# Optimization experiments

Hardware: AMD Instinct MI355X
Metric: run time of the kernel (lower is better)

## Reference

```python
import jax, jax.numpy as jnp
import numpy as np

B, C, L, E = 2048, 128, 16, 10      # atoms, channels, num_ell=(lmax+1)^2, elements
P3, P2, P1 = 23, 4, 1               # num CG paths per correlation order
U_DENSITY = 0.15                    # CG-like U tensors are highly sparse


def _sparse_u(key, shape):
    k1, k2 = jax.random.split(key)
    vals = jax.random.normal(k1, shape, dtype=jnp.float32)
    mask = jax.random.uniform(k2, shape) < U_DENSITY
    return jnp.where(mask, vals, 0.0)


def setup_inputs() -> dict:
    key = jax.random.key(0)
    ks = jax.random.split(key, 8)
    x = jax.random.normal(ks[0], (B, C, L), dtype=jnp.float32)
    y = jax.random.uniform(ks[1], (B, E), dtype=jnp.float32)  # element attrs
    U3 = _sparse_u(ks[2], (L, L, L, P3))
    U2 = _sparse_u(ks[3], (L, L, P2))
    U1 = _sparse_u(ks[4], (L, P1))
    W3 = jax.random.normal(ks[5], (E, P3, C), dtype=jnp.float32) / P3
    W2 = jax.random.normal(ks[6], (E, P2, C), dtype=jnp.float32) / P2
    W1 = jax.random.normal(ks[7], (E, P1, C), dtype=jnp.float32) / P1
    return {"x": x, "y": y, "U3": U3, "U2": U2, "U1": U1,
            "W3": W3, "W2": W2, "W1": W1}


def reference(x, y, U3, U2, U1, W3, W2, W1):
    # nu=3 main contraction: 'wxik,ekc,bci,be->bcwx'
    out = jnp.einsum('wxik,ekc,bci,be->bcwx', U3, W3, x, y, optimize='optimal')  # [B,C,L,L]
    # nu=2: weighting then feature contraction
    c2 = jnp.einsum('wxk,ekc,be->bcwx', U2, W2, y, optimize='optimal') + out
    out = jnp.einsum('bcwi,bci->bcw', c2, x)                                     # [B,C,L]
    # nu=1
    c1 = jnp.einsum('wk,ekc,be->bcw', U1, W1, y, optimize='optimal') + out
    out = jnp.einsum('bci,bci->bc', c1, x)                                       # [B,C]
    return out.reshape(out.shape[0], -1)
```

## Files before the change

kernel.cpp:

```cpp
#include <hip/hip_runtime.h>
#include <hip/hip_bf16.h>

typedef __attribute__((ext_vector_type(8))) short short8;
typedef __attribute__((ext_vector_type(4))) float f32x4;

#define LL 16
#define NP3 23
#define NE 10
#define NC 128
#define KI 24
#define KTOT 384
#define NSTEPS 12
#define MT 64
#define THREADS 512
#define WAVES 8
#define ZPAD 392

__global__ void build_B(const float* __restrict__ U3, const float* __restrict__ U2,
                        __hip_bfloat16* __restrict__ Bf) {
    int s    = blockIdx.x >> 4;
    int n16  = blockIdx.x & 15;
    int lane = threadIdx.x;
    int ar   = lane & 15, kg = lane >> 4;
    int n    = n16 * 16 + ar;
    __hip_bfloat16 vals[8];
#pragma unroll
    for (int j = 0; j < 8; ++j) {
        int kk = s * 32 + kg * 8 + j;
        int i  = kk / KI, k = kk - i * KI;
        float v;
        if (k < NP3)      v = U3[((size_t)n * LL + i) * NP3 + k];
        else if (i < 4)   v = U2[n * 4 + i];
        else              v = 0.f;
        vals[j] = __float2bfloat16(v);
    }
    *reinterpret_cast<short8*>(Bf + ((size_t)blockIdx.x * 64 + lane) * 8) =
        *reinterpret_cast<short8*>(vals);
}

__global__ __launch_bounds__(THREADS, 4)
void contract_k(const float* __restrict__ x, const float* __restrict__ y,
                const float* __restrict__ W3, const float* __restrict__ W2,
                const float* __restrict__ W1, const float* __restrict__ U1,
                const __hip_bfloat16* __restrict__ Bf, float* __restrict__ out) {
    __shared__ __align__(16) __hip_bfloat16 Zt[MT][ZPAD];
    __shared__ float xs[MT][17];
    __shared__ float wys[MT][28];
    __shared__ float part[MT][WAVES];

    const int tid = threadIdx.x;
    const int m0  = blockIdx.x * MT;

    for (int idx = tid; idx < MT * LL; idx += THREADS) {
        xs[idx >> 4][idx & 15] = x[(size_t)m0 * LL + idx];
    }

    {
        int r = tid >> 3, p = tid & 7;
        int m = m0 + r;
        int c = m & (NC - 1);
        const float* yr = y + (size_t)(m >> 7) * NE;
        float yv[NE];
#pragma unroll
        for (int e = 0; e < NE; ++e) yv[e] = yr[e];
#pragma unroll
        for (int j = 0; j < 4; ++j) {
            int idx = p * 4 + j;
            if (idx < 28) {
                float s = 0.f;
                if (idx < NP3) {
#pragma unroll
                    for (int e = 0; e < NE; ++e) s += yv[e] * W3[(e * NP3 + idx) * NC + c];
                } else if (idx < 27) {
                    int k2 = idx - NP3;
#pragma unroll
                    for (int e = 0; e < NE; ++e) s += yv[e] * W2[(e * 4 + k2) * NC + c];
                } else {
#pragma unroll
                    for (int e = 0; e < NE; ++e) s += yv[e] * W1[e * NC + c];
                }
                wys[r][idx] = s;
            }
        }
    }
    __syncthreads();

    {
        int r = tid >> 3, p = tid & 7;
        float wv[NP3];
#pragma unroll
        for (int k = 0; k < NP3; ++k) wv[k] = wys[r][k];
#pragma unroll
        for (int ii = 0; ii < 2; ++ii) {
            int i = p * 2 + ii;
            float xi   = xs[r][i];
            float slot = (i < 4) ? wys[r][NP3 + i] : 0.f;
            __hip_bfloat162* dst = reinterpret_cast<__hip_bfloat162*>(&Zt[r][i * KI]);
#pragma unroll
            for (int kp = 0; kp < 12; ++kp) {
                float a = xi * wv[2 * kp];
                float b = (kp < 11) ? xi * wv[2 * kp + 1] : slot;
                __hip_bfloat162 pk;
                pk.x = __float2bfloat16(a);
                pk.y = __float2bfloat16(b);
                dst[kp] = pk;
            }
        }
    }
    __syncthreads();

    const int lane = tid & 63;
    const int nw   = tid >> 6;
    const int ar   = lane & 15;
    const int kg   = lane >> 4;
    f32x4 acc[4][2];
#pragma unroll
    for (int mt = 0; mt < 4; ++mt)
#pragma unroll
        for (int nf = 0; nf < 2; ++nf) acc[mt][nf] = f32x4{0.f, 0.f, 0.f, 0.f};

    const short8* Bv = reinterpret_cast<const short8*>(Bf);
#pragma unroll
    for (int s = 0; s < NSTEPS; ++s) {
        short8 b0 = Bv[((size_t)(s * 16 + nw * 2 + 0)) * 64 + lane];
        short8 b1 = Bv[((size_t)(s * 16 + nw * 2 + 1)) * 64 + lane];
#pragma unroll
        for (int mt = 0; mt < 4; ++mt) {
            short8 a = *reinterpret_cast<const short8*>(&Zt[mt * 16 + ar][s * 32 + kg * 8]);
            acc[mt][0] = __builtin_amdgcn_mfma_f32_16x16x32_bf16(a, b0, acc[mt][0], 0, 0, 0);
            acc[mt][1] = __builtin_amdgcn_mfma_f32_16x16x32_bf16(a, b1, acc[mt][1], 0, 0, 0);
        }
    }

#pragma unroll
    for (int mt = 0; mt < 4; ++mt) {
#pragma unroll
        for (int q = 0; q < 4; ++q) {
            int row  = mt * 16 + kg * 4 + q;
            float xx = xs[row][ar];
            float sl = xx * (acc[mt][0][q] * xs[row][nw * 2] +
                             acc[mt][1][q] * xs[row][nw * 2 + 1]);
            sl += __shfl_xor(sl, 1);
            sl += __shfl_xor(sl, 2);
            sl += __shfl_xor(sl, 4);
            sl += __shfl_xor(sl, 8);
            if (ar == 0) part[row][nw] = sl;
        }
    }
    __syncthreads();

    if (tid < MT) {
        int r = tid;
        float s = 0.f;
#pragma unroll
        for (int w8 = 0; w8 < WAVES; ++w8) s += part[r][w8];
        float du = 0.f;
#pragma unroll
        for (int w = 0; w < LL; ++w) du += U1[w] * xs[r][w];
        out[m0 + r] = s + wys[r][27] * du;
    }
}

extern "C" void kernel_launch(void* const* d_in, const int* in_sizes, int n_in,
                              void* d_out, int out_size, void* d_ws, size_t ws_size,
                              hipStream_t stream) {
    const float* x  = (const float*)d_in[0];
    const float* y  = (const float*)d_in[1];
    const float* U3 = (const float*)d_in[2];
    const float* U2 = (const float*)d_in[3];
    const float* U1 = (const float*)d_in[4];
    const float* W3 = (const float*)d_in[5];
    const float* W2 = (const float*)d_in[6];
    const float* W1 = (const float*)d_in[7];
    __hip_bfloat16* Bf = (__hip_bfloat16*)d_ws;

    build_B<<<NSTEPS * 16, 64, 0, stream>>>(U3, U2, Bf);
    contract_k<<<4096, THREADS, 0, stream>>>(x, y, W3, W2, W1, U1, Bf, (float*)d_out);
}
```

Baseline: 131.6 us.

## Use 1024-thread blocks with one N-tile per wave and prefetched B fragments

Doubles the block to 16 waves so each wave handles a single 16-column N tile instead of two, which halves per-wave accumulators and MFMA count. The B fragment for the next K step is prefetched while the current step's MFMAs run. The wy precompute is re-indexed so consecutive threads read consecutive channels, each thread builds a whole Z row segment and writes it as 16-byte vector stores, and the partial-sum buffer now reuses Zt's shared memory, with an extra barrier added before that reuse. Per-block register pressure and a larger block size may limit occupancy, and xs loses its padding, which can cause LDS bank conflicts.

```diff
diff --git a/kernel.cpp b/kernel.cpp
--- a/kernel.cpp
+++ b/kernel.cpp
@@ -9,12 +9,11 @@
 #define NE 10
 #define NC 128
 #define KI 24
-#define KTOT 384
 #define NSTEPS 12
 #define MT 64
-#define THREADS 512
-#define WAVES 8
-#define ZPAD 392
+#define THREADS 1024
+#define NWAVES 16
+#define ZCOLS 392
 
 __global__ void build_B(const float* __restrict__ U3, const float* __restrict__ U2,
                         __hip_bfloat16* __restrict__ Bf) {
@@ -38,74 +37,61 @@
         *reinterpret_cast<short8*>(vals);
 }
 
-__global__ __launch_bounds__(THREADS, 4)
+__global__ __launch_bounds__(THREADS, 8)
 void contract_k(const float* __restrict__ x, const float* __restrict__ y,
                 const float* __restrict__ W3, const float* __restrict__ W2,
                 const float* __restrict__ W1, const float* __restrict__ U1,
                 const __hip_bfloat16* __restrict__ Bf, float* __restrict__ out) {
-    __shared__ __align__(16) __hip_bfloat16 Zt[MT][ZPAD];
-    __shared__ float xs[MT][17];
+    __shared__ __align__(16) __hip_bfloat16 Zt[MT][ZCOLS];
+    __shared__ float xs[MT][16];
     __shared__ float wys[MT][28];
-    __shared__ float part[MT][WAVES];
+    float (*part)[NWAVES] = reinterpret_cast<float (*)[NWAVES]>(&Zt[0][0]);
 
     const int tid = threadIdx.x;
     const int m0  = blockIdx.x * MT;
+    const int b   = m0 >> 7;
+    const int c0  = m0 & (NC - 1);
 
-    for (int idx = tid; idx < MT * LL; idx += THREADS) {
-        xs[idx >> 4][idx & 15] = x[(size_t)m0 * LL + idx];
-    }
+    xs[tid >> 4][tid & 15] = x[(size_t)m0 * LL + tid];
 
-    {
-        int r = tid >> 3, p = tid & 7;
-        int m = m0 + r;
-        int c = m & (NC - 1);
-        const float* yr = y + (size_t)(m >> 7) * NE;
-        float yv[NE];
+    float yv[NE];
 #pragma unroll
-        for (int e = 0; e < NE; ++e) yv[e] = yr[e];
+    for (int e = 0; e < NE; ++e) yv[e] = y[(size_t)b * NE + e];
+
+    for (int u = tid; u < 28 * MT; u += THREADS) {
+        int idx = u >> 6, r = u & 63;
+        int c = c0 + r;
+        float s = 0.f;
+        if (idx < NP3) {
 #pragma unroll
-        for (int j = 0; j < 4; ++j) {
-            int idx = p * 4 + j;
-            if (idx < 28) {
-                float s = 0.f;
-                if (idx < NP3) {
+            for (int e = 0; e < NE; ++e) s += yv[e] * W3[(e * NP3 + idx) * NC + c];
+        } else if (idx < 27) {
+            int k2 = idx - NP3;
 #pragma unroll
-                    for (int e = 0; e < NE; ++e) s += yv[e] * W3[(e * NP3 + idx) * NC + c];
-                } else if (idx < 27) {
-                    int k2 = idx - NP3;
+            for (int e = 0; e < NE; ++e) s += yv[e] * W2[(e * 4 + k2) * NC + c];
+        } else {
 #pragma unroll
-                    for (int e = 0; e < NE; ++e) s += yv[e] * W2[(e * 4 + k2) * NC + c];
-                } else {
-#pragma unroll
-                    for (int e = 0; e < NE; ++e) s += yv[e] * W1[e * NC + c];
-                }
-                wys[r][idx] = s;
-            }
+            for (int e = 0; e < NE; ++e) s += yv[e] * W1[e * NC + c];
         }
+        wys[r][idx] = s;
     }
     __syncthreads();
 
     {
-        int r = tid >> 3, p = tid & 7;
-        float wv[NP3];
+        int r = tid >> 4, i = tid & 15;
+        float xi = xs[r][i];
+        __hip_bfloat162 pk[12];
 #pragma unroll
-        for (int k = 0; k < NP3; ++k) wv[k] = wys[r][k];
-#pragma unroll
-        for (int ii = 0; ii < 2; ++ii) {
-            int i = p * 2 + ii;
-            float xi   = xs[r][i];
-            float slot = (i < 4) ? wys[r][NP3 + i] : 0.f;
-            __hip_bfloat162* dst = reinterpret_cast<__hip_bfloat162*>(&Zt[r][i * KI]);
-#pragma unroll
-            for (int kp = 0; kp < 12; ++kp) {
-                float a = xi * wv[2 * kp];
-                float b = (kp < 11) ? xi * wv[2 * kp + 1] : slot;
-                __hip_bfloat162 pk;
-                pk.x = __float2bfloat16(a);
-                pk.y = __float2bfloat16(b);
-                dst[kp] = pk;
-            }
+        for (int kp = 0; kp < 12; ++kp) {
+            float a  = xi * wys[r][2 * kp];
+            float bb = (kp < 11) ? xi * wys[r][2 * kp + 1]
+                                 : ((i < 4) ? wys[r][NP3 + i] : 0.f);
+            pk[kp].x = __float2bfloat16(a);
+            pk[kp].y = __float2bfloat16(bb);
         }
+        const short8* pv = reinterpret_cast<const short8*>(pk);
+        short8* dst = reinterpret_cast<short8*>(&Zt[r][i * KI]);
+        dst[0] = pv[0]; dst[1] = pv[1]; dst[2] = pv[2];
     }
     __syncthreads();
 
@@ -113,38 +99,36 @@
     const int nw   = tid >> 6;
     const int ar   = lane & 15;
     const int kg   = lane >> 4;
-    f32x4 acc[4][2];
+    f32x4 acc[4];
 #pragma unroll
-    for (int mt = 0; mt < 4; ++mt)
-#pragma unroll
-        for (int nf = 0; nf < 2; ++nf) acc[mt][nf] = f32x4{0.f, 0.f, 0.f, 0.f};
+    for (int mt = 0; mt < 4; ++mt) acc[mt] = f32x4{0.f, 0.f, 0.f, 0.f};
 
-    const short8* Bv = reinterpret_cast<const short8*>(Bf);
+    const short8* Bw = reinterpret_cast<const short8*>(Bf) + (size_t)nw * 64 + lane;
+    short8 bcur = Bw[0];
 #pragma unroll
     for (int s = 0; s < NSTEPS; ++s) {
-        short8 b0 = Bv[((size_t)(s * 16 + nw * 2 + 0)) * 64 + lane];
-        short8 b1 = Bv[((size_t)(s * 16 + nw * 2 + 1)) * 64 + lane];
+        short8 bnxt = bcur;
+        if (s + 1 < NSTEPS) bnxt = Bw[(size_t)(s + 1) * 1024];
 #pragma unroll
         for (int mt = 0; mt < 4; ++mt) {
             short8 a = *reinterpret_cast<const short8*>(&Zt[mt * 16 + ar][s * 32 + kg * 8]);
-            acc[mt][0] = __builtin_amdgcn_mfma_f32_16x16x32_bf16(a, b0, acc[mt][0], 0, 0, 0);
-            acc[mt][1] = __builtin_amdgcn_mfma_f32_16x16x32_bf16(a, b1, acc[mt][1], 0, 0, 0);
+            acc[mt] = __builtin_amdgcn_mfma_f32_16x16x32_bf16(a, bcur, acc[mt], 0, 0, 0);
         }
+        bcur = bnxt;
     }
+    __syncthreads();
 
 #pragma unroll
     for (int mt = 0; mt < 4; ++mt) {
 #pragma unroll
         for (int q = 0; q < 4; ++q) {
-            int row  = mt * 16 + kg * 4 + q;
-            float xx = xs[row][ar];
-            float sl = xx * (acc[mt][0][q] * xs[row][nw * 2] +
-                             acc[mt][1][q] * xs[row][nw * 2 + 1]);
+            int row = mt * 16 + kg * 4 + q;
+            float sl = acc[mt][q] * xs[row][ar];
             sl += __shfl_xor(sl, 1);
             sl += __shfl_xor(sl, 2);
             sl += __shfl_xor(sl, 4);
             sl += __shfl_xor(sl, 8);
-            if (ar == 0) part[row][nw] = sl;
+            if (ar == 0) part[row][nw] = xs[row][nw] * sl;
         }
     }
     __syncthreads();
@@ -153,7 +137,7 @@
         int r = tid;
         float s = 0.f;
 #pragma unroll
-        for (int w8 = 0; w8 < WAVES; ++w8) s += part[r][w8];
+        for (int w = 0; w < NWAVES; ++w) s += part[r][w];
         float du = 0.f;
 #pragma unroll
         for (int w = 0; w < LL; ++w) du += U1[w] * xs[r][w];
```

Result: faster. 126.9 us (-3.6%).
